# Kernel optimization log

Measured on AMD Instinct MI355X. Metric: run time of the kernel, lower is better.

The kernel has to match this reference:

```python
import jax, jax.numpy as jnp
import numpy as np

NUM_HEADS = 16
NUM_KV_HEADS = 4
HEAD_DIM = 128
ROPE_THETA = 10000.0


def _rope_cos_sin(T, dim, theta):
    inv_freq = 1.0 / (theta ** (jnp.arange(0, dim, 2, dtype=jnp.float32) / dim))
    freqs = jnp.arange(T, dtype=jnp.float32)[:, None] * inv_freq[None, :]  # (T, dim/2)
    emb = jnp.concatenate([freqs, freqs], axis=-1)  # (T, dim)
    return jnp.cos(emb), jnp.sin(emb)


def _rotate_half(x):
    h = x.shape[-1] // 2
    return jnp.concatenate([-x[..., h:], x[..., :h]], axis=-1)


def _apply_rope(x, cos, sin):
    # x: (B, H, T, D); cos/sin: (T, D)
    return x * cos[None, None] + _rotate_half(x) * sin[None, None]


def setup_inputs() -> dict:
    key = jax.random.key(0)
    ks = jax.random.split(key, 6)
    B, T, H = 2, 2048, 2048
    latent = 256
    kv_dim = NUM_KV_HEADS * HEAD_DIM
    s = 0.02
    return {
        "x": jax.random.normal(ks[0], (B, T, H), jnp.float32),
        "wq": jax.random.normal(ks[1], (H, H), jnp.float32) * s,
        "wkv": jax.random.normal(ks[2], (latent, H), jnp.float32) * s,
        "wk": jax.random.normal(ks[3], (kv_dim, latent), jnp.float32) * s,
        "wv": jax.random.normal(ks[4], (kv_dim, latent), jnp.float32) * s,
        "wo": jax.random.normal(ks[5], (H, H), jnp.float32) * s,
    }


def reference(x, wq, wkv, wk, wv, wo):
    B, T, hidden = x.shape
    nh, nkv, hd = NUM_HEADS, NUM_KV_HEADS, HEAD_DIM

    q = jnp.einsum('bth,dh->btd', x, wq)
    kv_latent = jnp.einsum('bth,lh->btl', x, wkv)
    k = jnp.einsum('btl,dl->btd', kv_latent, wk)
    v = jnp.einsum('btl,dl->btd', kv_latent, wv)

    q = q.reshape(B, T, nh, hd).transpose(0, 2, 1, 3)   # (B, nh, T, hd)
    k = k.reshape(B, T, nkv, hd).transpose(0, 2, 1, 3)  # (B, nkv, T, hd)
    v = v.reshape(B, T, nkv, hd).transpose(0, 2, 1, 3)

    cos, sin = _rope_cos_sin(T, hd, ROPE_THETA)
    q = _apply_rope(q, cos, sin)
    k = _apply_rope(k, cos, sin)

    rep = nh // nkv
    k = jnp.repeat(k, rep, axis=1)  # (B, nh, T, hd)
    v = jnp.repeat(v, rep, axis=1)

    scores = jnp.einsum('bhqd,bhkd->bhqk', q, k) * (1.0 / np.sqrt(hd))
    causal = jnp.triu(jnp.ones((T, T), dtype=bool), k=1)
    scores = jnp.where(causal[None, None], -jnp.inf, scores)
    probs = jax.nn.softmax(scores, axis=-1)
    out = jnp.einsum('bhqk,bhkd->bhqd', probs, v)
    out = out.transpose(0, 2, 1, 3).reshape(B, T, nh * hd)
    return jnp.einsum('btd,hd->bth', out, wo)
```

## Files before the change

kernel.cpp:

```cpp
#include <hip/hip_runtime.h>
#include <hip/hip_bf16.h>
#include <math.h>


#define AS1 __attribute__((address_space(1)))
#define AS3 __attribute__((address_space(3)))
#define QSTRIDE 2304

typedef short bf16x8 __attribute__((ext_vector_type(8)));
typedef float f32x4 __attribute__((ext_vector_type(4)));
typedef float f32x16 __attribute__((ext_vector_type(16)));
typedef unsigned int uint32x2 __attribute__((ext_vector_type(2)));

__device__ __forceinline__ unsigned short f2bf(float x) {
  union { float f; unsigned int u; } q; q.f = x;
  unsigned int u = q.u;
  u += 0x7FFFu + ((u >> 16) & 1u);
  return (unsigned short)(u >> 16);
}
__device__ __forceinline__ float bf2f(unsigned short x) {
  union { unsigned int u; float f; } q; q.u = ((unsigned int)x) << 16;
  return q.f;
}
__device__ __forceinline__ unsigned int pack2bf(float a, float b) {
  return (unsigned int)f2bf(a) | ((unsigned int)f2bf(b) << 16);
}
__device__ __forceinline__ unsigned int pack2bf_hw(float a, float b) {
  __hip_bfloat162 h = __float22bfloat162_rn(make_float2(a, b));
  union { __hip_bfloat162 h; unsigned int u; } c; c.h = h;
  return c.u;
}
__device__ __forceinline__ uint32x2 plswap(unsigned int a, unsigned int b) {
  return __builtin_amdgcn_permlane32_swap(a, b, false, false);
}
__device__ __forceinline__ float xor32_add(float x) {
  union { float f; unsigned int u; } X; X.f = x;
  uint32x2 r = plswap(X.u, X.u);
  union { unsigned int u; float f; } A, B; A.u = r.x; B.u = r.y;
  return A.f + B.f;
}

__global__ __launch_bounds__(256) void rope_table(float* __restrict__ cost,
                                                  float* __restrict__ sint,
                                                  int T) {
  int idx = blockIdx.x * 256 + threadIdx.x;
  if (idx >= T * 64) return;
  int t = idx >> 6, j = idx & 63;
  double invf = pow(10000.0, -(double)j / 64.0);
  double ang = (double)t * invf;
  cost[idx] = (float)cos(ang);
  sint[idx] = (float)sin(ang);
}

__global__ __launch_bounds__(256) void conv_all(const float* __restrict__ x,
                                                const float* __restrict__ wq,
                                                const float* __restrict__ wkv,
                                                const float* __restrict__ wk,
                                                const float* __restrict__ wv,
                                                const float* __restrict__ wo,
                                                unsigned short* __restrict__ dst) {
  const int b0 = 8388608;
  const int b1 = b0 + 4194304;
  const int b2 = b1 + 524288;
  const int b3 = b2 + 131072;
  const int b4 = b3 + 131072;
  const int b5 = b4 + 4194304;
  int i = (blockIdx.x * 256 + threadIdx.x) * 4;
  if (i >= b5) return;
  const float* src;
  int off;
  if (i < b0)      { src = x;   off = i; }
  else if (i < b1) { src = wq;  off = i - b0; }
  else if (i < b2) { src = wkv; off = i - b1; }
  else if (i < b3) { src = wk;  off = i - b2; }
  else if (i < b4) { src = wv;  off = i - b3; }
  else             { src = wo;  off = i - b4; }
  float4 f = *(const float4*)(src + off);
  ushort4 o;
  o.x = f2bf(f.x); o.y = f2bf(f.y); o.z = f2bf(f.z); o.w = f2bf(f.w);
  *(ushort4*)(dst + i) = o;
}

template <bool OUT_BF16>
__global__ __launch_bounds__(256) void gemm_mfma(const unsigned short* __restrict__ A,
                                                 const unsigned short* __restrict__ W,
                                                 void* __restrict__ Cv,
                                                 int M, int N, int K,
                                                 int lda, int ldw, int ldc,
                                                 int nwgx) {
  __shared__ unsigned short Asl[2][128 * 32];
  __shared__ unsigned short Wsl[2][128 * 32];
  int tid = threadIdx.x;
  int w = tid >> 6, lane = tid & 63;
  int g = lane >> 4, c = lane & 15;
  int wm = w >> 1, wn = w & 1;

  int nwg = gridDim.x;
  int cpx = nwg >> 3;
  int orig = blockIdx.x;
  int swz = (orig & 7) * cpx + (orig >> 3);
  int m0 = (swz / nwgx) * 128, n0 = (swz % nwgx) * 128;

  f32x4 acc[4][4] = {};

#pragma unroll
  for (int i = 0; i < 2; ++i) {
    int idx = i * 256 + tid;
    int row = idx >> 2;
    int kk = (idx & 3) * 8;
    __builtin_amdgcn_global_load_lds(
        (const AS1 void*)(A + (size_t)(m0 + row) * lda + kk),
        (AS3 void*)(Asl[0] + ((size_t)i * 256 + (w << 6)) * 8), 16, 0, 0);
    __builtin_amdgcn_global_load_lds(
        (const AS1 void*)(W + (size_t)(n0 + row) * ldw + kk),
        (AS3 void*)(Wsl[0] + ((size_t)i * 256 + (w << 6)) * 8), 16, 0, 0);
  }
  __syncthreads();

  int cur = 0;
  for (int k0 = 0; k0 < K; k0 += 32) {
    if (k0 + 32 < K) {
      int nb = cur ^ 1;
#pragma unroll
      for (int i = 0; i < 2; ++i) {
        int idx = i * 256 + tid;
        int row = idx >> 2;
        int kk = (idx & 3) * 8;
        __builtin_amdgcn_global_load_lds(
            (const AS1 void*)(A + (size_t)(m0 + row) * lda + k0 + 32 + kk),
            (AS3 void*)(Asl[nb] + ((size_t)i * 256 + (w << 6)) * 8), 16, 0, 0);
        __builtin_amdgcn_global_load_lds(
            (const AS1 void*)(W + (size_t)(n0 + row) * ldw + k0 + 32 + kk),
            (AS3 void*)(Wsl[nb] + ((size_t)i * 256 + (w << 6)) * 8), 16, 0, 0);
      }
    }
    bf16x8 af[4], wf[4];
#pragma unroll
    for (int mi = 0; mi < 4; ++mi)
      af[mi] = *(const bf16x8*)(Asl[cur] + (wm * 64 + mi * 16 + c) * 32 + g * 8);
#pragma unroll
    for (int ni = 0; ni < 4; ++ni)
      wf[ni] = *(const bf16x8*)(Wsl[cur] + (wn * 64 + ni * 16 + c) * 32 + g * 8);
#pragma unroll
    for (int mi = 0; mi < 4; ++mi)
#pragma unroll
      for (int ni = 0; ni < 4; ++ni)
        acc[mi][ni] = __builtin_amdgcn_mfma_f32_16x16x32_bf16(af[mi], wf[ni],
                                                              acc[mi][ni], 0, 0, 0);
    __syncthreads();
    cur ^= 1;
  }
#pragma unroll
  for (int mi = 0; mi < 4; ++mi)
#pragma unroll
    for (int r = 0; r < 4; ++r) {
      size_t mrow = (size_t)(m0 + wm * 64 + mi * 16 + g * 4 + r) * ldc;
#pragma unroll
      for (int ni = 0; ni < 4; ++ni) {
        int n = n0 + wn * 64 + ni * 16 + c;
        if (OUT_BF16)
          ((unsigned short*)Cv)[mrow + n] = f2bf(acc[mi][ni][r]);
        else
          ((float*)Cv)[mrow + n] = acc[mi][ni][r];
      }
    }
}

__global__ __launch_bounds__(256) void rope_ip_bf16(unsigned short* __restrict__ buf,
                                                    int nheads, int T, int rowstride,
                                                    const float* __restrict__ cost,
                                                    const float* __restrict__ sint,
                                                    float scale) {
  int idx = blockIdx.x * 256 + threadIdx.x;
  int d = idx & 63;
  int rest = idx >> 6;
  int h = rest % nheads;
  int bt = rest / nheads;
  int t = bt & (T - 1);
  unsigned short* p = buf + (size_t)bt * rowstride + h * 128;
  float cc = cost[t * 64 + d], ss = sint[t * 64 + d];
  float x0 = bf2f(p[d]), x1 = bf2f(p[d + 64]);
  p[d]      = f2bf((x0 * cc - x1 * ss) * scale);
  p[d + 64] = f2bf((x1 * cc + x0 * ss) * scale);
}

__global__ __launch_bounds__(256) void rope_pack_k(const unsigned short* __restrict__ kvcat,
                                                   unsigned short* __restrict__ kp,
                                                   const float* __restrict__ cost,
                                                   const float* __restrict__ sint) {
  int idx = blockIdx.x * 256 + threadIdx.x;
  int d = idx & 63;
  int rest = idx >> 6;
  int kvh = rest & 3;
  int bt = rest >> 2;
  int t = bt & 2047, b = bt >> 11;
  const unsigned short* src = kvcat + (size_t)bt * 1024 + kvh * 128;
  float cc = cost[t * 64 + d], ss = sint[t * 64 + d];
  float x0 = bf2f(src[d]), x1 = bf2f(src[d + 64]);
  unsigned short y0 = f2bf(x0 * cc - x1 * ss);
  unsigned short y1 = f2bf(x1 * cc + x0 * ss);
  int kr = t & 31;
  size_t base = (size_t)(b * 4 + kvh) * 262144 + (size_t)(t >> 5) * 4096;
  kp[base + ((kr * 128 + d)      ^ ((kr & 7) << 3))] = y0;
  kp[base + ((kr * 128 + d + 64) ^ ((kr & 7) << 3))] = y1;
}

__global__ __launch_bounds__(256) void transpose_v(const unsigned short* __restrict__ kvcat,
                                                   unsigned short* __restrict__ vp) {
  __shared__ unsigned short tile[32][33];
  int t0 = blockIdx.x * 32, d0 = blockIdx.y * 32, b = blockIdx.z;
  int tx = threadIdx.x & 31, ty = threadIdx.x >> 5;
#pragma unroll
  for (int i = 0; i < 4; ++i) {
    int t = ty + i * 8;
    tile[t][tx] = kvcat[((size_t)(b * 2048 + t0 + t)) * 1024 + 512 + d0 + tx];
  }
  __syncthreads();
#pragma unroll
  for (int i = 0; i < 4; ++i) {
    int dd = ty + i * 8;
    int D = d0 + dd;
    int d = D & 127;
    int t = t0 + tx;
    size_t base = (size_t)(b * 4 + (D >> 7)) * 262144 + (size_t)(t >> 5) * 4096;
    vp[base + ((d * 32 + (t & 31)) ^ ((d & 3) << 3))] = tile[tx][dd];
  }
}

__global__ __launch_bounds__(256, 2) void attn_mfma(const unsigned short* __restrict__ qb,
                                                    const unsigned short* __restrict__ kp,
                                                    const unsigned short* __restrict__ vp,
                                                    unsigned short* __restrict__ attob) {
  __shared__ unsigned short smem[16896];

  int tid = threadIdx.x;
  int w = tid >> 6, lane = tid & 63;
  int wq = w >> 1, wk = w & 1;
  int cl = lane & 31, hi = lane >> 5;
  int stream = blockIdx.x & 31;
  int G = 31 - (blockIdx.x >> 5);
  int h = stream & 15, b = stream >> 4;
  int kvh = h >> 2;
  int q0w = G * 64 + wq * 32;
  int nt = 2 * G + 2;

  const unsigned short* kpS = kp + (size_t)(b * 4 + kvh) * 262144;
  const unsigned short* vpS = vp + (size_t)(b * 4 + kvh) * 262144;

  bf16x8 qa[8];
  {
    const unsigned short* qrow = qb + ((size_t)(b * 2048 + q0w + cl)) * QSTRIDE + h * 128 + hi * 8;
#pragma unroll
    for (int kc = 0; kc < 8; ++kc)
      qa[kc] = *(const bf16x8*)(qrow + kc * 16);
  }

  f32x16 o0 = {}, o1 = {}, o2 = {}, o3 = {};
  float l = 0.f;

#pragma unroll
  for (int i = 0; i < 2; ++i) {
    __builtin_amdgcn_global_load_lds(
        (const AS1 void*)(kpS + (size_t)w * 1024 + i * 512 + lane * 8),
        (AS3 void*)(&smem[w * 1024 + i * 512]), 16, 0, 0);
    __builtin_amdgcn_global_load_lds(
        (const AS1 void*)(vpS + (size_t)w * 1024 + i * 512 + lane * 8),
        (AS3 void*)(&smem[8192 + w * 1024 + i * 512]), 16, 0, 0);
  }
  __syncthreads();

  int cur = 0;
  for (int ti = 0; ti < nt; ++ti) {
    if (ti + 1 < nt) {
      size_t src = (size_t)(ti + 1) * 4096 + w * 1024 + lane * 8;
      int nb = cur ^ 1;
#pragma unroll
      for (int i = 0; i < 2; ++i) {
        __builtin_amdgcn_global_load_lds(
            (const AS1 void*)(kpS + src + i * 512),
            (AS3 void*)(&smem[nb * 4096 + w * 1024 + i * 512]), 16, 0, 0);
        __builtin_amdgcn_global_load_lds(
            (const AS1 void*)(vpS + src + i * 512),
            (AS3 void*)(&smem[8192 + nb * 4096 + w * 1024 + i * 512]), 16, 0, 0);
      }
    }
    int ks0 = ti << 5;
    if (((ti & 1) == wk) && (ks0 <= q0w)) {
      const unsigned short* kb_ = &smem[cur * 4096];
      const unsigned short* vb_ = &smem[8192 + cur * 4096];
      bf16x8 kf[8];
#pragma unroll
      for (int kc = 0; kc < 8; ++kc)
        kf[kc] = *(const bf16x8*)&kb_[(cl * 128 + kc * 16 + hi * 8) ^ ((cl & 7) << 3)];
      f32x16 sA = {}, sB = {};
      __builtin_amdgcn_s_setprio(1);
#pragma unroll
      for (int kc = 0; kc < 4; ++kc) {
        sA = __builtin_amdgcn_mfma_f32_32x32x16_bf16(kf[kc * 2],     qa[kc * 2],     sA, 0, 0, 0);
        sB = __builtin_amdgcn_mfma_f32_32x32x16_bf16(kf[kc * 2 + 1], qa[kc * 2 + 1], sB, 0, 0, 0);
      }
      __builtin_amdgcn_s_setprio(0);
      f32x16 sS = sA + sB;
      bf16x8 vf[8];
#pragma unroll
      for (int db = 0; db < 4; ++db)
#pragma unroll
        for (int ks = 0; ks < 2; ++ks)
          vf[db * 2 + ks] = *(const bf16x8*)&vb_[((db * 32 + cl) * 32
                              + ks * 16 + hi * 8) ^ ((cl & 3) << 3)];
      if (ks0 == q0w) {
#pragma unroll
        for (int r = 0; r < 16; ++r) {
          int krow = (r & 3) + 8 * (r >> 2) + 4 * hi;
          if (krow > cl) sS[r] = -INFINITY;
        }
      }
      float p[16];
#pragma unroll
      for (int r = 0; r < 16; ++r) p[r] = __expf(sS[r]);
      float rs = ((p[0] + p[1]) + (p[2] + p[3])) + ((p[4] + p[5]) + (p[6] + p[7]))
               + ((p[8] + p[9]) + (p[10] + p[11])) + ((p[12] + p[13]) + (p[14] + p[15]));
      l += rs;
      union { unsigned int u[4]; bf16x8 v; } pb0, pb1;
      {
        uint32x2 r0 = plswap(pack2bf_hw(p[0], p[1]), pack2bf_hw(p[4], p[5]));
        uint32x2 r1 = plswap(pack2bf_hw(p[2], p[3]), pack2bf_hw(p[6], p[7]));
        pb0.u[0] = r0.x; pb0.u[1] = r1.x; pb0.u[2] = r0.y; pb0.u[3] = r1.y;
        uint32x2 r2 = plswap(pack2bf_hw(p[8], p[9]), pack2bf_hw(p[12], p[13]));
        uint32x2 r3 = plswap(pack2bf_hw(p[10], p[11]), pack2bf_hw(p[14], p[15]));
        pb1.u[0] = r2.x; pb1.u[1] = r3.x; pb1.u[2] = r2.y; pb1.u[3] = r3.y;
      }
      __builtin_amdgcn_s_setprio(1);
      o0 = __builtin_amdgcn_mfma_f32_32x32x16_bf16(vf[0], pb0.v, o0, 0, 0, 0);
      o1 = __builtin_amdgcn_mfma_f32_32x32x16_bf16(vf[2], pb0.v, o1, 0, 0, 0);
      o2 = __builtin_amdgcn_mfma_f32_32x32x16_bf16(vf[4], pb0.v, o2, 0, 0, 0);
      o3 = __builtin_amdgcn_mfma_f32_32x32x16_bf16(vf[6], pb0.v, o3, 0, 0, 0);
      o0 = __builtin_amdgcn_mfma_f32_32x32x16_bf16(vf[1], pb1.v, o0, 0, 0, 0);
      o1 = __builtin_amdgcn_mfma_f32_32x32x16_bf16(vf[3], pb1.v, o1, 0, 0, 0);
      o2 = __builtin_amdgcn_mfma_f32_32x32x16_bf16(vf[5], pb1.v, o2, 0, 0, 0);
      o3 = __builtin_amdgcn_mfma_f32_32x32x16_bf16(vf[7], pb1.v, o3, 0, 0, 0);
      __builtin_amdgcn_s_setprio(0);
    }
    __syncthreads();
    cur ^= 1;
  }

  float lsum = xor32_add(l);
  float* lptr = (float*)&smem[16384];
  int qr = wq * 32 + cl;
  if (hi == 0) lptr[wk * 64 + qr] = lsum;
#pragma unroll
  for (int r = 0; r < 16; ++r) {
    int dl = (r & 3) + 8 * (r >> 2) + 4 * hi;
    smem[wk * 8192 + qr * 128 + dl]      = f2bf(o0[r]);
    smem[wk * 8192 + qr * 128 + 32 + dl] = f2bf(o1[r]);
    smem[wk * 8192 + qr * 128 + 64 + dl] = f2bf(o2[r]);
    smem[wk * 8192 + qr * 128 + 96 + dl] = f2bf(o3[r]);
  }
  __syncthreads();

  {
    int q = tid >> 2;
    int dc = (tid & 3) * 32;
    float inv = 1.f / (lptr[q] + lptr[64 + q]);
    unsigned short* orow = attob + ((size_t)(b * 2048 + G * 64 + q)) * 2048 + h * 128 + dc;
#pragma unroll
    for (int i4 = 0; i4 < 4; ++i4) {
      bf16x8 a = *(const bf16x8*)&smem[q * 128 + dc + i4 * 8];
      bf16x8 c = *(const bf16x8*)&smem[8192 + q * 128 + dc + i4 * 8];
      union { unsigned int u[4]; bf16x8 v; } ov;
#pragma unroll
      for (int j = 0; j < 4; ++j) {
        float s0 = (bf2f((unsigned short)a[j * 2])     + bf2f((unsigned short)c[j * 2]))     * inv;
        float s1 = (bf2f((unsigned short)a[j * 2 + 1]) + bf2f((unsigned short)c[j * 2 + 1])) * inv;
        ov.u[j] = pack2bf(s0, s1);
      }
      *(bf16x8*)(orow + i4 * 8) = ov.v;
    }
  }
}

extern "C" void kernel_launch(void* const* d_in, const int* in_sizes, int n_in,
                              void* d_out, int out_size, void* d_ws, size_t ws_size,
                              hipStream_t stream) {
  const float* x   = (const float*)d_in[0];
  const float* wq  = (const float*)d_in[1];
  const float* wkv = (const float*)d_in[2];
  const float* wk  = (const float*)d_in[3];
  const float* wv  = (const float*)d_in[4];
  const float* wo  = (const float*)d_in[5];
  float* out = (float*)d_out;
  float* ws  = (float*)d_ws;

  const int B = 2, T = 2048, H = 2048, NH = 16, NKV = 4, LAT = 256, KVD = 512;
  const int BT = B * T;

  size_t off = 0;
  unsigned short* xb    = (unsigned short*)(ws + off); off += (size_t)BT * H / 2;
  unsigned short* wqb   = (unsigned short*)(ws + off); off += (size_t)H * H / 2;
  unsigned short* wkvb  = (unsigned short*)(ws + off); off += (size_t)LAT * H / 2;
  unsigned short* wkb   = (unsigned short*)(ws + off); off += (size_t)KVD * LAT / 2;
  unsigned short* wvb   = (unsigned short*)(ws + off); off += (size_t)KVD * LAT / 2;
  unsigned short* wob   = (unsigned short*)(ws + off); off += (size_t)H * H / 2;
  unsigned short* qkv   = (unsigned short*)(ws + off); off += (size_t)BT * QSTRIDE / 2;
  unsigned short* kvcat = (unsigned short*)(ws + off); off += (size_t)BT * 1024 / 2;
  unsigned short* kp    = (unsigned short*)(ws + off); off += (size_t)BT * KVD / 2;
  unsigned short* vp    = (unsigned short*)(ws + off); off += (size_t)BT * KVD / 2;
  unsigned short* attob = (unsigned short*)(ws + off); off += (size_t)BT * H / 2;
  float* cost = ws + off; off += (size_t)T * 64;
  float* sint = ws + off; off += (size_t)T * 64;

  const float scale = 0.088388347648318447f;

  rope_table<<<(T * 64 + 255) / 256, 256, 0, stream>>>(cost, sint, T);

  conv_all<<<17152, 256, 0, stream>>>(x, wq, wkv, wk, wv, wo, xb);

  gemm_mfma<true><<<(QSTRIDE / 128) * (BT / 128), 256, 0, stream>>>(
      xb, wqb, qkv, BT, QSTRIDE, H, H, H, QSTRIDE, QSTRIDE / 128);
  gemm_mfma<true><<<(1024 / 128) * (BT / 128), 256, 0, stream>>>(
      qkv + H, wkb, kvcat, BT, 1024, LAT, QSTRIDE, LAT, 1024, 1024 / 128);

  rope_ip_bf16<<<(BT * NH * 64) / 256, 256, 0, stream>>>(qkv, NH, T, QSTRIDE, cost, sint, scale);
  rope_pack_k<<<(BT * NKV * 64) / 256, 256, 0, stream>>>(kvcat, kp, cost, sint);
  transpose_v<<<dim3(T / 32, KVD / 32, B), 256, 0, stream>>>(kvcat, vp);

  attn_mfma<<<1024, 256, 0, stream>>>(qkv, kp, vp, attob);

  gemm_mfma<false><<<(H / 128) * (BT / 128), 256, 0, stream>>>(
      attob, wob, out, BT, H, H, H, H, H, H / 128);
}
```

Before: 215.4 us.

## Fuse RoPE, K packing and V transpose into GEMM epilogues

Applies rotary embedding and scaling to Q directly in the QKV GEMM epilogue, exchanging half-head partner values through shared memory. The K/V GEMM writes rotated, swizzled K and transposed V straight into the attention layouts. This drops three elementwise/transpose kernels and the intermediate kvcat round trip through global memory. In exchange it adds extra syncs and scattered 2-byte stores in the epilogue.

```diff
diff --git a/kernel.cpp b/kernel.cpp
--- a/kernel.cpp
+++ b/kernel.cpp
@@ -81,13 +81,18 @@
   *(ushort4*)(dst + i) = o;
 }
 
-template <bool OUT_BF16>
+template <int MODE>
 __global__ __launch_bounds__(256) void gemm_mfma(const unsigned short* __restrict__ A,
                                                  const unsigned short* __restrict__ W,
                                                  void* __restrict__ Cv,
                                                  int M, int N, int K,
                                                  int lda, int ldw, int ldc,
-                                                 int nwgx) {
+                                                 int nwgx,
+                                                 unsigned short* __restrict__ kp,
+                                                 unsigned short* __restrict__ vp,
+                                                 const float* __restrict__ cost,
+                                                 const float* __restrict__ sint,
+                                                 float scale) {
   __shared__ unsigned short Asl[2][128 * 32];
   __shared__ unsigned short Wsl[2][128 * 32];
   int tid = threadIdx.x;
@@ -150,80 +155,72 @@
     __syncthreads();
     cur ^= 1;
   }
-#pragma unroll
-  for (int mi = 0; mi < 4; ++mi)
-#pragma unroll
-    for (int r = 0; r < 4; ++r) {
-      size_t mrow = (size_t)(m0 + wm * 64 + mi * 16 + g * 4 + r) * ldc;
+
+  bool needRope = (MODE == 1 && n0 < 2048) || (MODE == 2 && n0 < 512);
+  if (needRope) {
+    float* X = (float*)Asl;
+#pragma unroll
+    for (int mi = 0; mi < 4; ++mi) {
+      __syncthreads();
+#pragma unroll
+      for (int ni = 0; ni < 4; ++ni)
+#pragma unroll
+        for (int r = 0; r < 4; ++r)
+          X[((((wm << 1) | wn) * 16) + (g * 4 + r)) * 64 + ni * 16 + c] = acc[mi][ni][r];
+      __syncthreads();
 #pragma unroll
       for (int ni = 0; ni < 4; ++ni) {
-        int n = n0 + wn * 64 + ni * 16 + c;
-        if (OUT_BF16)
-          ((unsigned short*)Cv)[mrow + n] = f2bf(acc[mi][ni][r]);
-        else
-          ((float*)Cv)[mrow + n] = acc[mi][ni][r];
+        int dlow = ni * 16 + c;
+#pragma unroll
+        for (int r = 0; r < 4; ++r) {
+          int row = m0 + wm * 64 + mi * 16 + g * 4 + r;
+          int t = row & 2047;
+          float part = X[((((wm << 1) | (wn ^ 1)) * 16) + (g * 4 + r)) * 64 + dlow];
+          float own = acc[mi][ni][r];
+          float cc = cost[t * 64 + dlow], ss = sint[t * 64 + dlow];
+          float val = (wn == 0) ? (own * cc - part * ss) : (own * cc + part * ss);
+          if (MODE == 1) {
+            ((unsigned short*)Cv)[(size_t)row * ldc + n0 + wn * 64 + dlow] = f2bf(val * scale);
+          } else {
+            int kvh = n0 >> 7;
+            int d = wn * 64 + dlow;
+            int kr = t & 31;
+            size_t base = (size_t)((row >> 11) * 4 + kvh) * 262144 + (size_t)(t >> 5) * 4096;
+            kp[base + ((kr * 128 + d) ^ ((kr & 7) << 3))] = f2bf(val);
+          }
+        }
       }
     }
-}
-
-__global__ __launch_bounds__(256) void rope_ip_bf16(unsigned short* __restrict__ buf,
-                                                    int nheads, int T, int rowstride,
-                                                    const float* __restrict__ cost,
-                                                    const float* __restrict__ sint,
-                                                    float scale) {
-  int idx = blockIdx.x * 256 + threadIdx.x;
-  int d = idx & 63;
-  int rest = idx >> 6;
-  int h = rest % nheads;
-  int bt = rest / nheads;
-  int t = bt & (T - 1);
-  unsigned short* p = buf + (size_t)bt * rowstride + h * 128;
-  float cc = cost[t * 64 + d], ss = sint[t * 64 + d];
-  float x0 = bf2f(p[d]), x1 = bf2f(p[d + 64]);
-  p[d]      = f2bf((x0 * cc - x1 * ss) * scale);
-  p[d + 64] = f2bf((x1 * cc + x0 * ss) * scale);
-}
-
-__global__ __launch_bounds__(256) void rope_pack_k(const unsigned short* __restrict__ kvcat,
-                                                   unsigned short* __restrict__ kp,
-                                                   const float* __restrict__ cost,
-                                                   const float* __restrict__ sint) {
-  int idx = blockIdx.x * 256 + threadIdx.x;
-  int d = idx & 63;
-  int rest = idx >> 6;
-  int kvh = rest & 3;
-  int bt = rest >> 2;
-  int t = bt & 2047, b = bt >> 11;
-  const unsigned short* src = kvcat + (size_t)bt * 1024 + kvh * 128;
-  float cc = cost[t * 64 + d], ss = sint[t * 64 + d];
-  float x0 = bf2f(src[d]), x1 = bf2f(src[d + 64]);
-  unsigned short y0 = f2bf(x0 * cc - x1 * ss);
-  unsigned short y1 = f2bf(x1 * cc + x0 * ss);
-  int kr = t & 31;
-  size_t base = (size_t)(b * 4 + kvh) * 262144 + (size_t)(t >> 5) * 4096;
-  kp[base + ((kr * 128 + d)      ^ ((kr & 7) << 3))] = y0;
-  kp[base + ((kr * 128 + d + 64) ^ ((kr & 7) << 3))] = y1;
-}
-
-__global__ __launch_bounds__(256) void transpose_v(const unsigned short* __restrict__ kvcat,
-                                                   unsigned short* __restrict__ vp) {
-  __shared__ unsigned short tile[32][33];
-  int t0 = blockIdx.x * 32, d0 = blockIdx.y * 32, b = blockIdx.z;
-  int tx = threadIdx.x & 31, ty = threadIdx.x >> 5;
-#pragma unroll
-  for (int i = 0; i < 4; ++i) {
-    int t = ty + i * 8;
-    tile[t][tx] = kvcat[((size_t)(b * 2048 + t0 + t)) * 1024 + 512 + d0 + tx];
-  }
-  __syncthreads();
-#pragma unroll
-  for (int i = 0; i < 4; ++i) {
-    int dd = ty + i * 8;
-    int D = d0 + dd;
-    int d = D & 127;
-    int t = t0 + tx;
-    size_t base = (size_t)(b * 4 + (D >> 7)) * 262144 + (size_t)(t >> 5) * 4096;
-    vp[base + ((d * 32 + (t & 31)) ^ ((d & 3) << 3))] = tile[tx][dd];
+  } else if (MODE == 2) {
+    int kvh = (n0 - 512) >> 7;
+#pragma unroll
+    for (int mi = 0; mi < 4; ++mi)
+#pragma unroll
+      for (int ni = 0; ni < 4; ++ni) {
+        int d = wn * 64 + ni * 16 + c;
+#pragma unroll
+        for (int r = 0; r < 4; ++r) {
+          int row = m0 + wm * 64 + mi * 16 + g * 4 + r;
+          int t = row & 2047;
+          size_t base = (size_t)((row >> 11) * 4 + kvh) * 262144 + (size_t)(t >> 5) * 4096;
+          vp[base + ((d * 32 + (t & 31)) ^ ((d & 3) << 3))] = f2bf(acc[mi][ni][r]);
+        }
+      }
+  } else {
+#pragma unroll
+    for (int mi = 0; mi < 4; ++mi)
+#pragma unroll
+      for (int r = 0; r < 4; ++r) {
+        size_t mrow = (size_t)(m0 + wm * 64 + mi * 16 + g * 4 + r) * ldc;
+#pragma unroll
+        for (int ni = 0; ni < 4; ++ni) {
+          int n = n0 + wn * 64 + ni * 16 + c;
+          if (MODE == 0)
+            ((float*)Cv)[mrow + n] = acc[mi][ni][r];
+          else
+            ((unsigned short*)Cv)[mrow + n] = f2bf(acc[mi][ni][r]);
+        }
+      }
   }
 }
 
@@ -409,6 +406,7 @@
   unsigned short* attob = (unsigned short*)(ws + off); off += (size_t)BT * H / 2;
   float* cost = ws + off; off += (size_t)T * 64;
   float* sint = ws + off; off += (size_t)T * 64;
+  (void)kvcat;
 
   const float scale = 0.088388347648318447f;
 
@@ -416,17 +414,16 @@
 
   conv_all<<<17152, 256, 0, stream>>>(x, wq, wkv, wk, wv, wo, xb);
 
-  gemm_mfma<true><<<(QSTRIDE / 128) * (BT / 128), 256, 0, stream>>>(
-      xb, wqb, qkv, BT, QSTRIDE, H, H, H, QSTRIDE, QSTRIDE / 128);
-  gemm_mfma<true><<<(1024 / 128) * (BT / 128), 256, 0, stream>>>(
-      qkv + H, wkb, kvcat, BT, 1024, LAT, QSTRIDE, LAT, 1024, 1024 / 128);
-
-  rope_ip_bf16<<<(BT * NH * 64) / 256, 256, 0, stream>>>(qkv, NH, T, QSTRIDE, cost, sint, scale);
-  rope_pack_k<<<(BT * NKV * 64) / 256, 256, 0, stream>>>(kvcat, kp, cost, sint);
-  transpose_v<<<dim3(T / 32, KVD / 32, B), 256, 0, stream>>>(kvcat, vp);
+  gemm_mfma<1><<<(QSTRIDE / 128) * (BT / 128), 256, 0, stream>>>(
+      xb, wqb, qkv, BT, QSTRIDE, H, H, H, QSTRIDE, QSTRIDE / 128,
+      nullptr, nullptr, cost, sint, scale);
+  gemm_mfma<2><<<(1024 / 128) * (BT / 128), 256, 0, stream>>>(
+      qkv + H, wkb, nullptr, BT, 1024, LAT, QSTRIDE, LAT, 1024, 1024 / 128,
+      kp, vp, cost, sint, 1.0f);
 
   attn_mfma<<<1024, 256, 0, stream>>>(qkv, kp, vp, attob);
 
-  gemm_mfma<false><<<(H / 128) * (BT / 128), 256, 0, stream>>>(
-      attob, wob, out, BT, H, H, H, H, H, H / 128);
-}
+  gemm_mfma<0><<<(H / 128) * (BT / 128), 256, 0, stream>>>(
+      attob, wob, out, BT, H, H, H, H, H, H / 128,
+      nullptr, nullptr, nullptr, nullptr, 1.0f);
+}
```

Result: slower. 222.0 us (+3.1%).
